# Optimization experiments

Measured on AMD Instinct MI355X. Metric: run time of the kernel, lower is better.

## Reference

```python
import jax, jax.numpy as jnp
import numpy as np


def setup_inputs() -> dict:
    key = jax.random.key(0)
    ks = jax.random.split(key, 4)
    B, N, C, S, D_AGG, D_OUT = 16, 2048, 128, 25, 128, 128
    # sparse binary adjacency, avg degree ~ N*0.01 ~ 20
    A = (jax.random.uniform(ks[0], (B, N, N)) < 0.01).astype(jnp.float32)
    X = jax.random.normal(ks[1], (B, N, C), dtype=jnp.float32)
    Wa = jax.random.normal(ks[2], (C, D_AGG), dtype=jnp.float32) * 0.05
    ba = jnp.zeros((D_AGG,), jnp.float32)
    Wc = jax.random.normal(ks[3], (C + D_AGG, D_OUT), dtype=jnp.float32) * 0.05
    bc = jnp.zeros((D_OUT,), jnp.float32)
    return {"A": A, "X": X, "Wa": Wa, "ba": ba, "Wc": Wc, "bc": bc, "n_samples": S}


def reference(A, X, Wa, ba, Wc, bc, n_samples):
    # Per node: take up to n_samples neighbors (nonzero adjacency entries).
    # Original randomly subsamples when degree > S; we take the first S by
    # index (lax.top_k is stable, ties -> lowest index). Missing slots are
    # zero rows, matching the original tf.pad: they contribute relu(ba) to
    # the max-aggregator, exactly like the padded/no-neighbor branches.
    mask = (A != 0).astype(X.dtype)                      # [B,N,N]
    vals, idx = jax.lax.top_k(mask, n_samples)           # [B,N,S]
    feats = jax.vmap(lambda x, i: jnp.take(x, i, axis=0))(X, idx)  # [B,N,S,C]
    feats = feats * vals[..., None]                      # zero padded slots
    # max aggregator: relu(neigh @ Wa + ba), max over sampled neighbors
    h = jax.nn.relu(jnp.einsum('bnsc,cd->bnsd', feats, Wa) + ba)
    agg = h.max(axis=2)                                  # [B,N,D_AGG]
    # concat self features with aggregated, project, relu
    cat = jnp.concatenate([X, agg], axis=-1)             # [B,N,C+D_AGG]
    out = jax.nn.relu(jnp.einsum('bnk,ko->bno', cat, Wc) + bc)  # [B,N,D_OUT]
    # per-graph Frobenius-norm normalization with div_no_nan semantics
    norm = jnp.sqrt(jnp.sum(out * out, axis=(1, 2), keepdims=True))
    return jnp.where(norm > 0, out / norm, jnp.zeros_like(out))
```

## Files before the change

### kernel.cpp

```cpp
#include <hip/hip_runtime.h>


typedef __attribute__((ext_vector_type(8))) short short8;
typedef __attribute__((ext_vector_type(4))) float f32x4;
typedef __attribute__((ext_vector_type(4))) float fvec4;
typedef unsigned int uint;
typedef unsigned short ushort;

__device__ __forceinline__ ushort f2bf(float x) {
    uint u = __builtin_bit_cast(uint, x);
    u += 0x7FFFu + ((u >> 16) & 1u);
    return (ushort)(u >> 16);
}
__device__ __forceinline__ float bflo(uint h) { uint v = h << 16;         return __builtin_bit_cast(float, v); }
__device__ __forceinline__ float bfhi(uint h) { uint v = h & 0xFFFF0000u; return __builtin_bit_cast(float, v); }

__global__ __launch_bounds__(256) void prep_w_k(
    const float* __restrict__ Wa, ushort* __restrict__ Wat,
    uint* __restrict__ ctr)
{
    int i = blockIdx.x * 256 + threadIdx.x;
    int d = i >> 7, k = i & 127;
    Wat[i] = f2bf(Wa[k * 128 + d]);
    if (i == 0) *ctr = 0u;
}

__device__ __forceinline__ void gemm_core(
    const float*  __restrict__ Xf, const ushort* __restrict__ A1,
    const ushort* __restrict__ Bt, int ktiles, int tile,
    ushort* Asm, ushort* Bsm, f32x4 acc[4][4])
{
    const int tid = threadIdx.x;
    const int l = tid & 63, w = tid >> 6;
    const int wm = (w >> 1) * 64, wn = (w & 1) * 64;
    const size_t row0 = (size_t)tile * 128;
    const int KT = ktiles << 7;

    for (int t = 0; t < ktiles; ++t) {
        __syncthreads();
        if (t == 0) {
#pragma unroll
            for (int j = 0; j < 8; ++j) {
                int gid = (j << 8) + tid;
                int r = gid >> 4, g = gid & 15;
                const float* s = Xf + (row0 + r) * 128 + g * 8;
                short8 pk;
#pragma unroll
                for (int e = 0; e < 8; ++e) pk[e] = (short)f2bf(s[e]);
                *(short8*)&Asm[r * 128 + ((g ^ (r & 7)) << 3)] = pk;
            }
        } else {
#pragma unroll
            for (int j = 0; j < 8; ++j) {
                int gid = (j << 8) + tid;
                int r = gid >> 4, g = gid & 15;
                short8 v = *(const short8*)(A1 + (row0 + r) * 128 + g * 8);
                *(short8*)&Asm[r * 128 + ((g ^ (r & 7)) << 3)] = v;
            }
        }
#pragma unroll
        for (int j = 0; j < 8; ++j) {
            int gid = (j << 8) + tid;
            int r = gid >> 4, g = gid & 15;
            short8 v = *(const short8*)(Bt + (size_t)r * KT + (t << 7) + g * 8);
            *(short8*)&Bsm[r * 128 + ((g ^ (r & 7)) << 3)] = v;
        }
        __syncthreads();
#pragma unroll
        for (int ks = 0; ks < 4; ++ks) {
            int gg = (ks << 2) + (l >> 4);
            short8 af[4], bfr[4];
#pragma unroll
            for (int m = 0; m < 4; ++m) {
                int r = wm + m * 16 + (l & 15);
                af[m] = *(const short8*)&Asm[r * 128 + ((gg ^ (r & 7)) << 3)];
            }
#pragma unroll
            for (int n = 0; n < 4; ++n) {
                int c = wn + n * 16 + (l & 15);
                bfr[n] = *(const short8*)&Bsm[c * 128 + ((gg ^ (c & 7)) << 3)];
            }
#pragma unroll
            for (int m = 0; m < 4; ++m)
#pragma unroll
                for (int n = 0; n < 4; ++n)
                    acc[m][n] = __builtin_amdgcn_mfma_f32_16x16x32_bf16(
                        af[m], bfr[n], acc[m][n], 0, 0, 0);
        }
    }
}

__global__ __launch_bounds__(256) void gemm_k1_k(
    const float* __restrict__ X, const ushort* __restrict__ Wat,
    const float* __restrict__ ba, ushort* __restrict__ H)
{
    __shared__ ushort Asm[128 * 128];
    __shared__ ushort Bsm[128 * 128];
    f32x4 acc[4][4] = {};
    gemm_core(X, nullptr, Wat, 1, blockIdx.x, Asm, Bsm, acc);

    const int tid = threadIdx.x, l = tid & 63, w = tid >> 6;
    const int wm = (w >> 1) * 64, wn = (w & 1) * 64;
    const size_t row0 = (size_t)blockIdx.x * 128;
    float bcol[4];
#pragma unroll
    for (int n = 0; n < 4; ++n) bcol[n] = ba[wn + n * 16 + (l & 15)];
#pragma unroll
    for (int m = 0; m < 4; ++m) {
        int rbase = wm + m * 16 + ((l >> 4) << 2);
#pragma unroll
        for (int n = 0; n < 4; ++n) {
            int col = wn + n * 16 + (l & 15);
#pragma unroll
            for (int r = 0; r < 4; ++r) {
                float v = fmaxf(acc[m][n][r] + bcol[n], 0.f);
                H[(row0 + rbase + r) * 128 + col] = f2bf(v);
            }
        }
    }
}

__global__ __launch_bounds__(256) void agg_k(
    const float* __restrict__ A,
    const uint*  __restrict__ Hu,
    const float* __restrict__ ba,
    uint* __restrict__ aggu,
    const int* __restrict__ nsp,
    const float* __restrict__ Wc,
    ushort* __restrict__ Wct)
{
    if (blockIdx.x >= 8192) {
        int j = (blockIdx.x - 8192) * 256 + threadIdx.x;
        int d = j >> 8, k = j & 255;
        Wct[j] = f2bf(Wc[k * 128 + d]);
        return;
    }

    __shared__ int idxs[4][32];
    const int l = threadIdx.x & 63;
    const int w = threadIdx.x >> 6;
    const int bid   = blockIdx.x;
    const int xcd   = bid & 7;
    const int grp   = bid >> 3;
    const int batch = ((grp >> 9) << 3) + xcd;
    const int node  = (batch << 11) + ((grp & 511) << 2) + w;
    int S = nsp[0]; if (S > 32) S = 32;

    const fvec4* rowp = (const fvec4*)(A + (size_t)node * 2048);
    fvec4 v[8];
#pragma unroll
    for (int c = 0; c < 8; ++c)
        v[c] = __builtin_nontemporal_load(rowp + c * 64 + l);

    const unsigned long long lt = (1ull << l) - 1ull;
    int base = 0;
#pragma unroll
    for (int c = 0; c < 8; ++c) {
        if (base < S) {
            unsigned long long m0 = __ballot(v[c][0] != 0.f);
            unsigned long long m1 = __ballot(v[c][1] != 0.f);
            unsigned long long m2 = __ballot(v[c][2] != 0.f);
            unsigned long long m3 = __ballot(v[c][3] != 0.f);
            int below = __popcll(m0 & lt) + __popcll(m1 & lt)
                      + __popcll(m2 & lt) + __popcll(m3 & lt);
            int o0 = (int)((m0 >> l) & 1), o1 = (int)((m1 >> l) & 1);
            int o2 = (int)((m2 >> l) & 1), o3 = (int)((m3 >> l) & 1);
            int r0 = base + below;
            int r1 = r0 + o0, r2 = r1 + o1, r3 = r2 + o2;
            int e = (c << 8) + (l << 2);
            if (o0 && r0 < S) idxs[w][r0] = e;
            if (o1 && r1 < S) idxs[w][r1] = e + 1;
            if (o2 && r2 < S) idxs[w][r2] = e + 2;
            if (o3 && r3 < S) idxs[w][r3] = e + 3;
            base += __popcll(m0) + __popcll(m1) + __popcll(m2) + __popcll(m3);
        }
    }
    int found = base < S ? base : S;

    float i0 = fmaxf(ba[2 * l], 0.f), i1 = fmaxf(ba[2 * l + 1], 0.f);
    float r0f = i0, r1f = i1;
    if (found > 0) {
        int fill = idxs[w][0];
        if (l < 32)
            idxs[w][l] = (l < found) ? idxs[w][l] : fill;

        const uint* HB = Hu + ((size_t)batch << 17);
        uint h[32];
#pragma unroll
        for (int q = 0; q < 32; ++q)
            h[q] = HB[(size_t)idxs[w][q] * 64 + l];

        float a0[8], a1[8];
#pragma unroll
        for (int q = 0; q < 8; ++q) { a0[q] = i0; a1[q] = i1; }
#pragma unroll
        for (int q = 0; q < 32; ++q) {
            a0[q & 7] = fmaxf(a0[q & 7], bflo(h[q]));
            a1[q & 7] = fmaxf(a1[q & 7], bfhi(h[q]));
        }
#pragma unroll
        for (int q = 0; q < 4; ++q) {
            a0[q] = fmaxf(a0[q], a0[q + 4]);
            a1[q] = fmaxf(a1[q], a1[q + 4]);
        }
        r0f = fmaxf(fmaxf(a0[0], a0[1]), fmaxf(a0[2], a0[3]));
        r1f = fmaxf(fmaxf(a1[0], a1[1]), fmaxf(a1[2], a1[3]));
    }
    aggu[(size_t)node * 64 + l] = (uint)f2bf(r0f) | ((uint)f2bf(r1f) << 16);
}

__global__ __launch_bounds__(256) void gemm_k3_k(
    const float* __restrict__ X, const ushort* __restrict__ agg,
    const ushort* __restrict__ Wct, const float* __restrict__ bc,
    float* __restrict__ out, float* __restrict__ partials,
    uint* __restrict__ ctr)
{
    __shared__ ushort Asm[128 * 128];
    __shared__ ushort Bsm[128 * 128];
    __shared__ float wred[4];
    __shared__ float ssc;
    f32x4 acc[4][4] = {};
    const int tile = blockIdx.x;
    gemm_core(X, agg, Wct, 2, tile, Asm, Bsm, acc);

    const int tid = threadIdx.x, l = tid & 63, w = tid >> 6;
    const int wm = (w >> 1) * 64, wn = (w & 1) * 64;
    const size_t row0 = (size_t)tile * 128;

    float bcol[4];
#pragma unroll
    for (int n = 0; n < 4; ++n) bcol[n] = bc[wn + n * 16 + (l & 15)];
    float lsum = 0.f;
#pragma unroll
    for (int m = 0; m < 4; ++m)
#pragma unroll
        for (int n = 0; n < 4; ++n)
#pragma unroll
            for (int r = 0; r < 4; ++r) {
                float v = fmaxf(acc[m][n][r] + bcol[n], 0.f);
                acc[m][n][r] = v;
                lsum += v * v;
            }
#pragma unroll
    for (int off = 32; off > 0; off >>= 1) lsum += __shfl_down(lsum, off);
    if (l == 0) wred[w] = lsum;
    __syncthreads();
    if (tid == 0) {
        partials[tile] = wred[0] + wred[1] + wred[2] + wred[3];
        __threadfence();
        __hip_atomic_fetch_add(ctr, 1u, __ATOMIC_ACQ_REL,
                               __HIP_MEMORY_SCOPE_AGENT);
        while (__hip_atomic_load(ctr, __ATOMIC_ACQUIRE,
                                 __HIP_MEMORY_SCOPE_AGENT) < 256u)
            __builtin_amdgcn_s_sleep(8);
        float s = 0.f;
        const int bb = tile >> 4;
#pragma unroll
        for (int i = 0; i < 16; ++i)
            s += __hip_atomic_load(&partials[bb * 16 + i], __ATOMIC_RELAXED,
                                   __HIP_MEMORY_SCOPE_AGENT);
        float norm = sqrtf(s);
        ssc = (norm > 0.f) ? (1.f / norm) : 0.f;
    }
    __syncthreads();
    const float sc = ssc;
#pragma unroll
    for (int m = 0; m < 4; ++m) {
        int rbase = wm + m * 16 + ((l >> 4) << 2);
#pragma unroll
        for (int n = 0; n < 4; ++n) {
            int col = wn + n * 16 + (l & 15);
#pragma unroll
            for (int r = 0; r < 4; ++r)
                out[(row0 + rbase + r) * 128 + col] = acc[m][n][r] * sc;
        }
    }
}

extern "C" void kernel_launch(void* const* d_in, const int* in_sizes, int n_in,
                              void* d_out, int out_size, void* d_ws, size_t ws_size,
                              hipStream_t stream) {
    const float* A  = (const float*)d_in[0];
    const float* X  = (const float*)d_in[1];
    const float* Wa = (const float*)d_in[2];
    const float* ba = (const float*)d_in[3];
    const float* Wc = (const float*)d_in[4];
    const float* bc = (const float*)d_in[5];
    const int*  nsp = (const int*)d_in[6];

    float* out = (float*)d_out;
    char* ws = (char*)d_ws;
    ushort* H        = (ushort*)ws;
    ushort* agg      = (ushort*)(ws + (8u << 20));
    ushort* Wat      = (ushort*)(ws + (16u << 20));
    ushort* Wct      = (ushort*)(ws + (16u << 20) + 32768);
    float*  partials = (float*) (ws + (16u << 20) + 131072);
    uint*   ctr      = (uint*)  (ws + (16u << 20) + 132096);

    prep_w_k<<<64, 256, 0, stream>>>(Wa, Wat, ctr);
    gemm_k1_k<<<256, 256, 0, stream>>>(X, Wat, ba, H);
    agg_k<<<8192 + 128, 256, 0, stream>>>(A, (const uint*)H, ba, (uint*)agg,
                                          nsp, Wc, Wct);
    gemm_k3_k<<<256, 256, 0, stream>>>(X, agg, Wct, bc, out, partials, ctr);
}
```

Before: 90.68 us.

## Fuse GEMM1, aggregation and GEMM2 into one persistent kernel with grid barriers

Replaces the three main kernels with a single persistent kernel of 512 blocks over 64-row tiles. Grid-wide atomic barriers separate the H projection, the neighbor max-aggregation and the output GEMM with norm. The aggregation now loops over 16 nodes per wave and prefetches the next adjacency row while gathering H. The aim is to remove launch gaps and tail effects, at the cost of fewer blocks streaming the 256MB adjacency (less memory-level parallelism) and three spin barriers.

```diff
diff --git a/kernel.cpp b/kernel.cpp
--- a/kernel.cpp
+++ b/kernel.cpp
@@ -15,32 +15,50 @@
 __device__ __forceinline__ float bflo(uint h) { uint v = h << 16;         return __builtin_bit_cast(float, v); }
 __device__ __forceinline__ float bfhi(uint h) { uint v = h & 0xFFFF0000u; return __builtin_bit_cast(float, v); }
 
-__global__ __launch_bounds__(256) void prep_w_k(
-    const float* __restrict__ Wa, ushort* __restrict__ Wat,
-    uint* __restrict__ ctr)
+__global__ __launch_bounds__(256) void prep_k(
+    const float* __restrict__ Wa, const float* __restrict__ Wc,
+    ushort* __restrict__ Wat, ushort* __restrict__ Wct, uint* __restrict__ ctr)
 {
     int i = blockIdx.x * 256 + threadIdx.x;
-    int d = i >> 7, k = i & 127;
-    Wat[i] = f2bf(Wa[k * 128 + d]);
-    if (i == 0) *ctr = 0u;
-}
-
-__device__ __forceinline__ void gemm_core(
+    if (i < 16384) {
+        int d = i >> 7, k = i & 127;
+        Wat[i] = f2bf(Wa[k * 128 + d]);
+    } else {
+        int j = i - 16384;
+        int d = j >> 8, k = j & 255;
+        Wct[j] = f2bf(Wc[k * 128 + d]);
+    }
+    if (blockIdx.x == 0 && threadIdx.x < 4) ctr[threadIdx.x] = 0u;
+}
+
+__device__ __forceinline__ void gbar(uint* c, int tid) {
+    __syncthreads();
+    if (tid == 0) {
+        __threadfence();
+        __hip_atomic_fetch_add(c, 1u, __ATOMIC_ACQ_REL,
+                               __HIP_MEMORY_SCOPE_AGENT);
+        while (__hip_atomic_load(c, __ATOMIC_ACQUIRE,
+                                 __HIP_MEMORY_SCOPE_AGENT) < 512u)
+            __builtin_amdgcn_s_sleep(4);
+    }
+    __syncthreads();
+    __threadfence();
+}
+
+__device__ __forceinline__ void gemm64(
     const float*  __restrict__ Xf, const ushort* __restrict__ A1,
-    const ushort* __restrict__ Bt, int ktiles, int tile,
-    ushort* Asm, ushort* Bsm, f32x4 acc[4][4])
+    const ushort* __restrict__ Bt, int KT, int ktiles, int tile64,
+    int tid, ushort* Asm, ushort* Bsm, f32x4 acc[4][2])
 {
-    const int tid = threadIdx.x;
     const int l = tid & 63, w = tid >> 6;
-    const int wm = (w >> 1) * 64, wn = (w & 1) * 64;
-    const size_t row0 = (size_t)tile * 128;
-    const int KT = ktiles << 7;
+    const int wn = w * 32;
+    const size_t row0 = (size_t)tile64 * 64;
 
     for (int t = 0; t < ktiles; ++t) {
         __syncthreads();
         if (t == 0) {
 #pragma unroll
-            for (int j = 0; j < 8; ++j) {
+            for (int j = 0; j < 4; ++j) {
                 int gid = (j << 8) + tid;
                 int r = gid >> 4, g = gid & 15;
                 const float* s = Xf + (row0 + r) * 128 + g * 8;
@@ -51,7 +69,7 @@
             }
         } else {
 #pragma unroll
-            for (int j = 0; j < 8; ++j) {
+            for (int j = 0; j < 4; ++j) {
                 int gid = (j << 8) + tid;
                 int r = gid >> 4, g = gid & 15;
                 short8 v = *(const short8*)(A1 + (row0 + r) * 128 + g * 8);
@@ -61,204 +79,191 @@
 #pragma unroll
         for (int j = 0; j < 8; ++j) {
             int gid = (j << 8) + tid;
-            int r = gid >> 4, g = gid & 15;
-            short8 v = *(const short8*)(Bt + (size_t)r * KT + (t << 7) + g * 8);
-            *(short8*)&Bsm[r * 128 + ((g ^ (r & 7)) << 3)] = v;
+            int c = gid >> 4, g = gid & 15;
+            short8 v = *(const short8*)(Bt + (size_t)c * KT + (t << 7) + g * 8);
+            *(short8*)&Bsm[c * 128 + ((g ^ (c & 7)) << 3)] = v;
         }
         __syncthreads();
 #pragma unroll
         for (int ks = 0; ks < 4; ++ks) {
             int gg = (ks << 2) + (l >> 4);
-            short8 af[4], bfr[4];
+            short8 af[4], bfr[2];
 #pragma unroll
             for (int m = 0; m < 4; ++m) {
-                int r = wm + m * 16 + (l & 15);
+                int r = m * 16 + (l & 15);
                 af[m] = *(const short8*)&Asm[r * 128 + ((gg ^ (r & 7)) << 3)];
             }
 #pragma unroll
-            for (int n = 0; n < 4; ++n) {
+            for (int n = 0; n < 2; ++n) {
                 int c = wn + n * 16 + (l & 15);
                 bfr[n] = *(const short8*)&Bsm[c * 128 + ((gg ^ (c & 7)) << 3)];
             }
 #pragma unroll
             for (int m = 0; m < 4; ++m)
 #pragma unroll
-                for (int n = 0; n < 4; ++n)
+                for (int n = 0; n < 2; ++n)
                     acc[m][n] = __builtin_amdgcn_mfma_f32_16x16x32_bf16(
                         af[m], bfr[n], acc[m][n], 0, 0, 0);
         }
     }
 }
 
-__global__ __launch_bounds__(256) void gemm_k1_k(
-    const float* __restrict__ X, const ushort* __restrict__ Wat,
-    const float* __restrict__ ba, ushort* __restrict__ H)
+__global__ __launch_bounds__(256, 2) void mega_k(
+    const float* __restrict__ A, const float* __restrict__ X,
+    const ushort* __restrict__ Wat, const ushort* __restrict__ Wct,
+    const float* __restrict__ ba, const float* __restrict__ bc,
+    ushort* __restrict__ H, uint* __restrict__ aggu,
+    float* __restrict__ out, float* __restrict__ partials,
+    uint* __restrict__ ctr, const int* __restrict__ nsp)
 {
-    __shared__ ushort Asm[128 * 128];
-    __shared__ ushort Bsm[128 * 128];
-    f32x4 acc[4][4] = {};
-    gemm_core(X, nullptr, Wat, 1, blockIdx.x, Asm, Bsm, acc);
-
-    const int tid = threadIdx.x, l = tid & 63, w = tid >> 6;
-    const int wm = (w >> 1) * 64, wn = (w & 1) * 64;
-    const size_t row0 = (size_t)blockIdx.x * 128;
-    float bcol[4];
-#pragma unroll
-    for (int n = 0; n < 4; ++n) bcol[n] = ba[wn + n * 16 + (l & 15)];
-#pragma unroll
-    for (int m = 0; m < 4; ++m) {
-        int rbase = wm + m * 16 + ((l >> 4) << 2);
-#pragma unroll
-        for (int n = 0; n < 4; ++n) {
-            int col = wn + n * 16 + (l & 15);
-#pragma unroll
-            for (int r = 0; r < 4; ++r) {
-                float v = fmaxf(acc[m][n][r] + bcol[n], 0.f);
-                H[(row0 + rbase + r) * 128 + col] = f2bf(v);
-            }
-        }
-    }
-}
-
-__global__ __launch_bounds__(256) void agg_k(
-    const float* __restrict__ A,
-    const uint*  __restrict__ Hu,
-    const float* __restrict__ ba,
-    uint* __restrict__ aggu,
-    const int* __restrict__ nsp,
-    const float* __restrict__ Wc,
-    ushort* __restrict__ Wct)
-{
-    if (blockIdx.x >= 8192) {
-        int j = (blockIdx.x - 8192) * 256 + threadIdx.x;
-        int d = j >> 8, k = j & 255;
-        Wct[j] = f2bf(Wc[k * 128 + d]);
-        return;
-    }
-
-    __shared__ int idxs[4][32];
-    const int l = threadIdx.x & 63;
-    const int w = threadIdx.x >> 6;
-    const int bid   = blockIdx.x;
-    const int xcd   = bid & 7;
-    const int grp   = bid >> 3;
-    const int batch = ((grp >> 9) << 3) + xcd;
-    const int node  = (batch << 11) + ((grp & 511) << 2) + w;
-    int S = nsp[0]; if (S > 32) S = 32;
-
-    const fvec4* rowp = (const fvec4*)(A + (size_t)node * 2048);
-    fvec4 v[8];
-#pragma unroll
-    for (int c = 0; c < 8; ++c)
-        v[c] = __builtin_nontemporal_load(rowp + c * 64 + l);
-
-    const unsigned long long lt = (1ull << l) - 1ull;
-    int base = 0;
-#pragma unroll
-    for (int c = 0; c < 8; ++c) {
-        if (base < S) {
-            unsigned long long m0 = __ballot(v[c][0] != 0.f);
-            unsigned long long m1 = __ballot(v[c][1] != 0.f);
-            unsigned long long m2 = __ballot(v[c][2] != 0.f);
-            unsigned long long m3 = __ballot(v[c][3] != 0.f);
-            int below = __popcll(m0 & lt) + __popcll(m1 & lt)
-                      + __popcll(m2 & lt) + __popcll(m3 & lt);
-            int o0 = (int)((m0 >> l) & 1), o1 = (int)((m1 >> l) & 1);
-            int o2 = (int)((m2 >> l) & 1), o3 = (int)((m3 >> l) & 1);
-            int r0 = base + below;
-            int r1 = r0 + o0, r2 = r1 + o1, r3 = r2 + o2;
-            int e = (c << 8) + (l << 2);
-            if (o0 && r0 < S) idxs[w][r0] = e;
-            if (o1 && r1 < S) idxs[w][r1] = e + 1;
-            if (o2 && r2 < S) idxs[w][r2] = e + 2;
-            if (o3 && r3 < S) idxs[w][r3] = e + 3;
-            base += __popcll(m0) + __popcll(m1) + __popcll(m2) + __popcll(m3);
-        }
-    }
-    int found = base < S ? base : S;
-
-    float i0 = fmaxf(ba[2 * l], 0.f), i1 = fmaxf(ba[2 * l + 1], 0.f);
-    float r0f = i0, r1f = i1;
-    if (found > 0) {
-        int fill = idxs[w][0];
-        if (l < 32)
-            idxs[w][l] = (l < found) ? idxs[w][l] : fill;
-
-        const uint* HB = Hu + ((size_t)batch << 17);
-        uint h[32];
-#pragma unroll
-        for (int q = 0; q < 32; ++q)
-            h[q] = HB[(size_t)idxs[w][q] * 64 + l];
-
-        float a0[8], a1[8];
-#pragma unroll
-        for (int q = 0; q < 8; ++q) { a0[q] = i0; a1[q] = i1; }
-#pragma unroll
-        for (int q = 0; q < 32; ++q) {
-            a0[q & 7] = fmaxf(a0[q & 7], bflo(h[q]));
-            a1[q & 7] = fmaxf(a1[q & 7], bfhi(h[q]));
-        }
-#pragma unroll
-        for (int q = 0; q < 4; ++q) {
-            a0[q] = fmaxf(a0[q], a0[q + 4]);
-            a1[q] = fmaxf(a1[q], a1[q + 4]);
-        }
-        r0f = fmaxf(fmaxf(a0[0], a0[1]), fmaxf(a0[2], a0[3]));
-        r1f = fmaxf(fmaxf(a1[0], a1[1]), fmaxf(a1[2], a1[3]));
-    }
-    aggu[(size_t)node * 64 + l] = (uint)f2bf(r0f) | ((uint)f2bf(r1f) << 16);
-}
-
-__global__ __launch_bounds__(256) void gemm_k3_k(
-    const float* __restrict__ X, const ushort* __restrict__ agg,
-    const ushort* __restrict__ Wct, const float* __restrict__ bc,
-    float* __restrict__ out, float* __restrict__ partials,
-    uint* __restrict__ ctr)
-{
-    __shared__ ushort Asm[128 * 128];
+    __shared__ ushort Asm[64 * 128];
     __shared__ ushort Bsm[128 * 128];
     __shared__ float wred[4];
     __shared__ float ssc;
-    f32x4 acc[4][4] = {};
-    const int tile = blockIdx.x;
-    gemm_core(X, agg, Wct, 2, tile, Asm, Bsm, acc);
 
     const int tid = threadIdx.x, l = tid & 63, w = tid >> 6;
-    const int wm = (w >> 1) * 64, wn = (w & 1) * 64;
-    const size_t row0 = (size_t)tile * 128;
-
-    float bcol[4];
-#pragma unroll
-    for (int n = 0; n < 4; ++n) bcol[n] = bc[wn + n * 16 + (l & 15)];
-    float lsum = 0.f;
-#pragma unroll
-    for (int m = 0; m < 4; ++m)
-#pragma unroll
-        for (int n = 0; n < 4; ++n)
-#pragma unroll
-            for (int r = 0; r < 4; ++r) {
-                float v = fmaxf(acc[m][n][r] + bcol[n], 0.f);
-                acc[m][n][r] = v;
-                lsum += v * v;
-            }
-#pragma unroll
-    for (int off = 32; off > 0; off >>= 1) lsum += __shfl_down(lsum, off);
-    if (l == 0) wred[w] = lsum;
-    __syncthreads();
+    const int bid = blockIdx.x;
+    const int xcd = bid & 7, rk = bid >> 3;
+    const int b_blk = (rk < 32) ? xcd : xcd + 8;
+    const int rk2 = rk & 31;
+    const int tile64 = b_blk * 32 + rk2;
+    const int wn = w * 32;
+    const size_t row0 = (size_t)tile64 * 64;
+
+    {
+        f32x4 acc[4][2] = {};
+        gemm64(X, nullptr, Wat, 128, 1, tile64, tid, Asm, Bsm, acc);
+        float bcol[2];
+#pragma unroll
+        for (int n = 0; n < 2; ++n) bcol[n] = ba[wn + n * 16 + (l & 15)];
+#pragma unroll
+        for (int m = 0; m < 4; ++m) {
+            int rbase = m * 16 + ((l >> 4) << 2);
+#pragma unroll
+            for (int n = 0; n < 2; ++n) {
+                int col = wn + n * 16 + (l & 15);
+#pragma unroll
+                for (int r = 0; r < 4; ++r)
+                    H[(row0 + rbase + r) * 128 + col] =
+                        f2bf(fmaxf(acc[m][n][r] + bcol[n], 0.f));
+            }
+        }
+    }
+    gbar(&ctr[0], tid);
+
+    {
+        int S = nsp[0]; if (S > 32) S = 32;
+        int* idxs = (int*)Asm;
+        const uint* HB = (const uint*)H + ((size_t)b_blk << 17);
+        const float i0 = fmaxf(ba[2 * l], 0.f), i1 = fmaxf(ba[2 * l + 1], 0.f);
+        const unsigned long long lt = (1ull << l) - 1ull;
+        const int nodeb = (b_blk << 11) + (rk2 << 6);
+
+        fvec4 v[8];
+        {
+            const fvec4* rp = (const fvec4*)(A + (size_t)(nodeb + w) * 2048);
+#pragma unroll
+            for (int c = 0; c < 8; ++c)
+                v[c] = __builtin_nontemporal_load(rp + c * 64 + l);
+        }
+        for (int i = 0; i < 16; ++i) {
+            const int node = nodeb + i * 4 + w;
+            int base = 0;
+#pragma unroll
+            for (int c = 0; c < 8; ++c) {
+                if (base < S) {
+                    unsigned long long m0 = __ballot(v[c][0] != 0.f);
+                    unsigned long long m1 = __ballot(v[c][1] != 0.f);
+                    unsigned long long m2 = __ballot(v[c][2] != 0.f);
+                    unsigned long long m3 = __ballot(v[c][3] != 0.f);
+                    int below = __popcll(m0 & lt) + __popcll(m1 & lt)
+                              + __popcll(m2 & lt) + __popcll(m3 & lt);
+                    int o0 = (int)((m0 >> l) & 1), o1 = (int)((m1 >> l) & 1);
+                    int o2 = (int)((m2 >> l) & 1), o3 = (int)((m3 >> l) & 1);
+                    int r0 = base + below;
+                    int r1 = r0 + o0, r2 = r1 + o1, r3 = r2 + o2;
+                    int e = (c << 8) + (l << 2);
+                    if (o0 && r0 < S) idxs[w * 32 + r0] = e;
+                    if (o1 && r1 < S) idxs[w * 32 + r1] = e + 1;
+                    if (o2 && r2 < S) idxs[w * 32 + r2] = e + 2;
+                    if (o3 && r3 < S) idxs[w * 32 + r3] = e + 3;
+                    base += __popcll(m0) + __popcll(m1)
+                          + __popcll(m2) + __popcll(m3);
+                }
+            }
+            const int found = base < S ? base : S;
+            const bool have = found > 0;
+
+            uint h[32];
+            if (have) {
+                int fill = idxs[w * 32];
+                if (l < 32)
+                    idxs[w * 32 + l] = (l < found) ? idxs[w * 32 + l] : fill;
+#pragma unroll
+                for (int q = 0; q < 32; ++q)
+                    h[q] = HB[(size_t)idxs[w * 32 + q] * 64 + l];
+            }
+            if (i < 15) {
+                const fvec4* rp =
+                    (const fvec4*)(A + (size_t)(nodeb + (i + 1) * 4 + w) * 2048);
+#pragma unroll
+                for (int c = 0; c < 8; ++c)
+                    v[c] = __builtin_nontemporal_load(rp + c * 64 + l);
+            }
+            float r0f = i0, r1f = i1;
+            if (have) {
+                float a0[8], a1[8];
+#pragma unroll
+                for (int q = 0; q < 8; ++q) { a0[q] = i0; a1[q] = i1; }
+#pragma unroll
+                for (int q = 0; q < 32; ++q) {
+                    a0[q & 7] = fmaxf(a0[q & 7], bflo(h[q]));
+                    a1[q & 7] = fmaxf(a1[q & 7], bfhi(h[q]));
+                }
+#pragma unroll
+                for (int q = 0; q < 4; ++q) {
+                    a0[q] = fmaxf(a0[q], a0[q + 4]);
+                    a1[q] = fmaxf(a1[q], a1[q + 4]);
+                }
+                r0f = fmaxf(fmaxf(a0[0], a0[1]), fmaxf(a0[2], a0[3]));
+                r1f = fmaxf(fmaxf(a1[0], a1[1]), fmaxf(a1[2], a1[3]));
+            }
+            aggu[(size_t)node * 64 + l] =
+                (uint)f2bf(r0f) | ((uint)f2bf(r1f) << 16);
+        }
+    }
+    gbar(&ctr[1], tid);
+
+    f32x4 acc[4][2] = {};
+    gemm64(X, (const ushort*)aggu, Wct, 256, 2, tile64, tid, Asm, Bsm, acc);
+    {
+        float bcol[2];
+#pragma unroll
+        for (int n = 0; n < 2; ++n) bcol[n] = bc[wn + n * 16 + (l & 15)];
+        float lsum = 0.f;
+#pragma unroll
+        for (int m = 0; m < 4; ++m)
+#pragma unroll
+            for (int n = 0; n < 2; ++n)
+#pragma unroll
+                for (int r = 0; r < 4; ++r) {
+                    float vv = fmaxf(acc[m][n][r] + bcol[n], 0.f);
+                    acc[m][n][r] = vv;
+                    lsum += vv * vv;
+                }
+#pragma unroll
+        for (int off = 32; off > 0; off >>= 1) lsum += __shfl_down(lsum, off);
+        if (l == 0) wred[w] = lsum;
+        __syncthreads();
+        if (tid == 0)
+            partials[tile64] = wred[0] + wred[1] + wred[2] + wred[3];
+    }
+    gbar(&ctr[2], tid);
+
     if (tid == 0) {
-        partials[tile] = wred[0] + wred[1] + wred[2] + wred[3];
-        __threadfence();
-        __hip_atomic_fetch_add(ctr, 1u, __ATOMIC_ACQ_REL,
-                               __HIP_MEMORY_SCOPE_AGENT);
-        while (__hip_atomic_load(ctr, __ATOMIC_ACQUIRE,
-                                 __HIP_MEMORY_SCOPE_AGENT) < 256u)
-            __builtin_amdgcn_s_sleep(8);
         float s = 0.f;
-        const int bb = tile >> 4;
-#pragma unroll
-        for (int i = 0; i < 16; ++i)
-            s += __hip_atomic_load(&partials[bb * 16 + i], __ATOMIC_RELAXED,
-                                   __HIP_MEMORY_SCOPE_AGENT);
+#pragma unroll
+        for (int i = 0; i < 32; ++i) s += partials[b_blk * 32 + i];
         float norm = sqrtf(s);
         ssc = (norm > 0.f) ? (1.f / norm) : 0.f;
     }
@@ -266,9 +271,9 @@
     const float sc = ssc;
 #pragma unroll
     for (int m = 0; m < 4; ++m) {
-        int rbase = wm + m * 16 + ((l >> 4) << 2);
-#pragma unroll
-        for (int n = 0; n < 4; ++n) {
+        int rbase = m * 16 + ((l >> 4) << 2);
+#pragma unroll
+        for (int n = 0; n < 2; ++n) {
             int col = wn + n * 16 + (l & 15);
 #pragma unroll
             for (int r = 0; r < 4; ++r)
@@ -291,15 +296,13 @@
     float* out = (float*)d_out;
     char* ws = (char*)d_ws;
     ushort* H        = (ushort*)ws;
-    ushort* agg      = (ushort*)(ws + (8u << 20));
+    uint*   agg      = (uint*)  (ws + (8u << 20));
     ushort* Wat      = (ushort*)(ws + (16u << 20));
     ushort* Wct      = (ushort*)(ws + (16u << 20) + 32768);
     float*  partials = (float*) (ws + (16u << 20) + 131072);
-    uint*   ctr      = (uint*)  (ws + (16u << 20) + 132096);
-
-    prep_w_k<<<64, 256, 0, stream>>>(Wa, Wat, ctr);
-    gemm_k1_k<<<256, 256, 0, stream>>>(X, Wat, ba, H);
-    agg_k<<<8192 + 128, 256, 0, stream>>>(A, (const uint*)H, ba, (uint*)agg,
-                                          nsp, Wc, Wct);
-    gemm_k3_k<<<256, 256, 0, stream>>>(X, agg, Wct, bc, out, partials, ctr);
-}
+    uint*   ctr      = (uint*)  (ws + (16u << 20) + 133120);
+
+    prep_k<<<192, 256, 0, stream>>>(Wa, Wc, Wat, Wct, ctr);
+    mega_k<<<512, 256, 0, stream>>>(A, X, Wat, Wct, ba, bc,
+                                    H, agg, out, partials, ctr, nsp);
+}
```

Measured after the change: 350.8 us. 287% more time.

## Split aggregation into independent scan and gather kernels, fold Wa transpose into GEMM

Applied to the files above, without the earlier changes.

Removes the separate weight-prep kernel by converting and transposing Wa directly inside the first GEMM. The fused aggregation kernel becomes two kernels. A scan kernel reads the adjacency and writes 16-bit global neighbor indices, with a sentinel row in H holding relu(ba) for nodes that have no neighbors. A gather kernel then does the max-reduction. The scan no longer depends on H, which may let the adjacency streaming run more independently of the first GEMM. The cost is an extra launch and an index buffer round-trip through memory.

```diff
diff --git a/kernel.cpp b/kernel.cpp
--- a/kernel.cpp
+++ b/kernel.cpp
@@ -15,93 +15,63 @@
 __device__ __forceinline__ float bflo(uint h) { uint v = h << 16;         return __builtin_bit_cast(float, v); }
 __device__ __forceinline__ float bfhi(uint h) { uint v = h & 0xFFFF0000u; return __builtin_bit_cast(float, v); }
 
-__global__ __launch_bounds__(256) void prep_w_k(
-    const float* __restrict__ Wa, ushort* __restrict__ Wat,
-    uint* __restrict__ ctr)
-{
-    int i = blockIdx.x * 256 + threadIdx.x;
-    int d = i >> 7, k = i & 127;
-    Wat[i] = f2bf(Wa[k * 128 + d]);
-    if (i == 0) *ctr = 0u;
-}
-
-__device__ __forceinline__ void gemm_core(
-    const float*  __restrict__ Xf, const ushort* __restrict__ A1,
-    const ushort* __restrict__ Bt, int ktiles, int tile,
-    ushort* Asm, ushort* Bsm, f32x4 acc[4][4])
-{
-    const int tid = threadIdx.x;
-    const int l = tid & 63, w = tid >> 6;
-    const int wm = (w >> 1) * 64, wn = (w & 1) * 64;
-    const size_t row0 = (size_t)tile * 128;
-    const int KT = ktiles << 7;
-
-    for (int t = 0; t < ktiles; ++t) {
-        __syncthreads();
-        if (t == 0) {
-#pragma unroll
-            for (int j = 0; j < 8; ++j) {
-                int gid = (j << 8) + tid;
-                int r = gid >> 4, g = gid & 15;
-                const float* s = Xf + (row0 + r) * 128 + g * 8;
-                short8 pk;
-#pragma unroll
-                for (int e = 0; e < 8; ++e) pk[e] = (short)f2bf(s[e]);
-                *(short8*)&Asm[r * 128 + ((g ^ (r & 7)) << 3)] = pk;
-            }
-        } else {
-#pragma unroll
-            for (int j = 0; j < 8; ++j) {
-                int gid = (j << 8) + tid;
-                int r = gid >> 4, g = gid & 15;
-                short8 v = *(const short8*)(A1 + (row0 + r) * 128 + g * 8);
-                *(short8*)&Asm[r * 128 + ((g ^ (r & 7)) << 3)] = v;
-            }
-        }
-#pragma unroll
-        for (int j = 0; j < 8; ++j) {
-            int gid = (j << 8) + tid;
-            int r = gid >> 4, g = gid & 15;
-            short8 v = *(const short8*)(Bt + (size_t)r * KT + (t << 7) + g * 8);
-            *(short8*)&Bsm[r * 128 + ((g ^ (r & 7)) << 3)] = v;
-        }
-        __syncthreads();
-#pragma unroll
-        for (int ks = 0; ks < 4; ++ks) {
-            int gg = (ks << 2) + (l >> 4);
-            short8 af[4], bfr[4];
-#pragma unroll
-            for (int m = 0; m < 4; ++m) {
-                int r = wm + m * 16 + (l & 15);
-                af[m] = *(const short8*)&Asm[r * 128 + ((gg ^ (r & 7)) << 3)];
-            }
-#pragma unroll
-            for (int n = 0; n < 4; ++n) {
-                int c = wn + n * 16 + (l & 15);
-                bfr[n] = *(const short8*)&Bsm[c * 128 + ((gg ^ (c & 7)) << 3)];
-            }
-#pragma unroll
-            for (int m = 0; m < 4; ++m)
-#pragma unroll
-                for (int n = 0; n < 4; ++n)
-                    acc[m][n] = __builtin_amdgcn_mfma_f32_16x16x32_bf16(
-                        af[m], bfr[n], acc[m][n], 0, 0, 0);
-        }
-    }
-}
-
 __global__ __launch_bounds__(256) void gemm_k1_k(
-    const float* __restrict__ X, const ushort* __restrict__ Wat,
+    const float* __restrict__ X, const float* __restrict__ Wa,
     const float* __restrict__ ba, ushort* __restrict__ H)
 {
     __shared__ ushort Asm[128 * 128];
     __shared__ ushort Bsm[128 * 128];
-    f32x4 acc[4][4] = {};
-    gemm_core(X, nullptr, Wat, 1, blockIdx.x, Asm, Bsm, acc);
-
     const int tid = threadIdx.x, l = tid & 63, w = tid >> 6;
     const int wm = (w >> 1) * 64, wn = (w & 1) * 64;
     const size_t row0 = (size_t)blockIdx.x * 128;
+
+#pragma unroll
+    for (int j = 0; j < 8; ++j) {
+        int gid = (j << 8) + tid;
+        int r = gid >> 4, g = gid & 15;
+        const float* s = X + (row0 + r) * 128 + g * 8;
+        short8 pk;
+#pragma unroll
+        for (int e = 0; e < 8; ++e) pk[e] = (short)f2bf(s[e]);
+        *(short8*)&Asm[r * 128 + ((g ^ (r & 7)) << 3)] = pk;
+    }
+    {
+        int c = tid >> 1;
+        int g0 = (tid & 1) * 8;
+#pragma unroll
+        for (int g = g0; g < g0 + 8; ++g) {
+            short8 pk;
+#pragma unroll
+            for (int e = 0; e < 8; ++e)
+                pk[e] = (short)f2bf(Wa[(size_t)(g * 8 + e) * 128 + c]);
+            *(short8*)&Bsm[c * 128 + ((g ^ (c & 7)) << 3)] = pk;
+        }
+    }
+    __syncthreads();
+
+    f32x4 acc[4][4] = {};
+#pragma unroll
+    for (int ks = 0; ks < 4; ++ks) {
+        int gg = (ks << 2) + (l >> 4);
+        short8 af[4], bfr[4];
+#pragma unroll
+        for (int m = 0; m < 4; ++m) {
+            int r = wm + m * 16 + (l & 15);
+            af[m] = *(const short8*)&Asm[r * 128 + ((gg ^ (r & 7)) << 3)];
+        }
+#pragma unroll
+        for (int n = 0; n < 4; ++n) {
+            int c = wn + n * 16 + (l & 15);
+            bfr[n] = *(const short8*)&Bsm[c * 128 + ((gg ^ (c & 7)) << 3)];
+        }
+#pragma unroll
+        for (int m = 0; m < 4; ++m)
+#pragma unroll
+            for (int n = 0; n < 4; ++n)
+                acc[m][n] = __builtin_amdgcn_mfma_f32_16x16x32_bf16(
+                    af[m], bfr[n], acc[m][n], 0, 0, 0);
+    }
+
     float bcol[4];
 #pragma unroll
     for (int n = 0; n < 4; ++n) bcol[n] = ba[wn + n * 16 + (l & 15)];
@@ -112,38 +82,39 @@
         for (int n = 0; n < 4; ++n) {
             int col = wn + n * 16 + (l & 15);
 #pragma unroll
-            for (int r = 0; r < 4; ++r) {
-                float v = fmaxf(acc[m][n][r] + bcol[n], 0.f);
-                H[(row0 + rbase + r) * 128 + col] = f2bf(v);
-            }
-        }
-    }
-}
-
-__global__ __launch_bounds__(256) void agg_k(
+            for (int r = 0; r < 4; ++r)
+                H[(row0 + rbase + r) * 128 + col] =
+                    f2bf(fmaxf(acc[m][n][r] + bcol[n], 0.f));
+        }
+    }
+    if (blockIdx.x == 0 && tid < 64) {
+        float a = fmaxf(ba[2 * tid], 0.f), b = fmaxf(ba[2 * tid + 1], 0.f);
+        ((uint*)(H + (size_t)32768 * 128))[tid] =
+            (uint)f2bf(a) | ((uint)f2bf(b) << 16);
+    }
+}
+
+__global__ __launch_bounds__(256) void scan_k(
     const float* __restrict__ A,
-    const uint*  __restrict__ Hu,
-    const float* __restrict__ ba,
-    uint* __restrict__ aggu,
+    ushort* __restrict__ idxg,
     const int* __restrict__ nsp,
     const float* __restrict__ Wc,
-    ushort* __restrict__ Wct)
+    ushort* __restrict__ Wct,
+    uint* __restrict__ ctr)
 {
     if (blockIdx.x >= 8192) {
         int j = (blockIdx.x - 8192) * 256 + threadIdx.x;
         int d = j >> 8, k = j & 255;
         Wct[j] = f2bf(Wc[k * 128 + d]);
+        if (blockIdx.x == 8192 && threadIdx.x == 0) *ctr = 0u;
         return;
     }
 
     __shared__ int idxs[4][32];
     const int l = threadIdx.x & 63;
     const int w = threadIdx.x >> 6;
-    const int bid   = blockIdx.x;
-    const int xcd   = bid & 7;
-    const int grp   = bid >> 3;
-    const int batch = ((grp >> 9) << 3) + xcd;
-    const int node  = (batch << 11) + ((grp & 511) << 2) + w;
+    const int node = blockIdx.x * 4 + w;
+    const int gbase = node & ~2047;
     int S = nsp[0]; if (S > 32) S = 32;
 
     const fvec4* rowp = (const fvec4*)(A + (size_t)node * 2048);
@@ -167,7 +138,7 @@
             int o2 = (int)((m2 >> l) & 1), o3 = (int)((m3 >> l) & 1);
             int r0 = base + below;
             int r1 = r0 + o0, r2 = r1 + o1, r3 = r2 + o2;
-            int e = (c << 8) + (l << 2);
+            int e = gbase + (c << 8) + (l << 2);
             if (o0 && r0 < S) idxs[w][r0] = e;
             if (o1 && r1 < S) idxs[w][r1] = e + 1;
             if (o2 && r2 < S) idxs[w][r2] = e + 2;
@@ -176,36 +147,52 @@
         }
     }
     int found = base < S ? base : S;
+    int fill = (found > 0) ? idxs[w][0] : 32768;
+    if (l < 32)
+        idxg[(size_t)node * 32 + l] =
+            (ushort)((l < found) ? idxs[w][l] : fill);
+}
+
+__global__ __launch_bounds__(256) void gather_k(
+    const ushort* __restrict__ idxg,
+    const uint*  __restrict__ Hu,
+    const float* __restrict__ ba,
+    uint* __restrict__ aggu)
+{
+    __shared__ ushort sidx[128];
+    const int l = threadIdx.x & 63;
+    const int w = threadIdx.x >> 6;
+    const int bid = blockIdx.x, xcd = bid & 7, grp = bid >> 3;
+    const int batch = ((grp >> 9) << 3) + xcd;
+    const int node0 = (batch << 11) + ((grp & 511) << 2);
+    const int node = node0 + w;
+
+    if (threadIdx.x < 64)
+        ((uint*)sidx)[threadIdx.x] =
+            ((const uint*)(idxg + (size_t)node0 * 32))[threadIdx.x];
+    __syncthreads();
+
+    uint h[32];
+#pragma unroll
+    for (int q = 0; q < 32; ++q)
+        h[q] = Hu[(size_t)sidx[w * 32 + q] * 64 + l];
 
     float i0 = fmaxf(ba[2 * l], 0.f), i1 = fmaxf(ba[2 * l + 1], 0.f);
-    float r0f = i0, r1f = i1;
-    if (found > 0) {
-        int fill = idxs[w][0];
-        if (l < 32)
-            idxs[w][l] = (l < found) ? idxs[w][l] : fill;
-
-        const uint* HB = Hu + ((size_t)batch << 17);
-        uint h[32];
-#pragma unroll
-        for (int q = 0; q < 32; ++q)
-            h[q] = HB[(size_t)idxs[w][q] * 64 + l];
-
-        float a0[8], a1[8];
-#pragma unroll
-        for (int q = 0; q < 8; ++q) { a0[q] = i0; a1[q] = i1; }
-#pragma unroll
-        for (int q = 0; q < 32; ++q) {
-            a0[q & 7] = fmaxf(a0[q & 7], bflo(h[q]));
-            a1[q & 7] = fmaxf(a1[q & 7], bfhi(h[q]));
-        }
-#pragma unroll
-        for (int q = 0; q < 4; ++q) {
-            a0[q] = fmaxf(a0[q], a0[q + 4]);
-            a1[q] = fmaxf(a1[q], a1[q + 4]);
-        }
-        r0f = fmaxf(fmaxf(a0[0], a0[1]), fmaxf(a0[2], a0[3]));
-        r1f = fmaxf(fmaxf(a1[0], a1[1]), fmaxf(a1[2], a1[3]));
-    }
+    float a0[8], a1[8];
+#pragma unroll
+    for (int q = 0; q < 8; ++q) { a0[q] = i0; a1[q] = i1; }
+#pragma unroll
+    for (int q = 0; q < 32; ++q) {
+        a0[q & 7] = fmaxf(a0[q & 7], bflo(h[q]));
+        a1[q & 7] = fmaxf(a1[q & 7], bfhi(h[q]));
+    }
+#pragma unroll
+    for (int q = 0; q < 4; ++q) {
+        a0[q] = fmaxf(a0[q], a0[q + 4]);
+        a1[q] = fmaxf(a1[q], a1[q + 4]);
+    }
+    float r0f = fmaxf(fmaxf(a0[0], a0[1]), fmaxf(a0[2], a0[3]));
+    float r1f = fmaxf(fmaxf(a1[0], a1[1]), fmaxf(a1[2], a1[3]));
     aggu[(size_t)node * 64 + l] = (uint)f2bf(r0f) | ((uint)f2bf(r1f) << 16);
 }
 
@@ -219,13 +206,64 @@
     __shared__ ushort Bsm[128 * 128];
     __shared__ float wred[4];
     __shared__ float ssc;
-    f32x4 acc[4][4] = {};
-    const int tile = blockIdx.x;
-    gemm_core(X, agg, Wct, 2, tile, Asm, Bsm, acc);
-
     const int tid = threadIdx.x, l = tid & 63, w = tid >> 6;
     const int wm = (w >> 1) * 64, wn = (w & 1) * 64;
+    const int tile = blockIdx.x;
     const size_t row0 = (size_t)tile * 128;
+
+    f32x4 acc[4][4] = {};
+    for (int t = 0; t < 2; ++t) {
+        __syncthreads();
+        if (t == 0) {
+#pragma unroll
+            for (int j = 0; j < 8; ++j) {
+                int gid = (j << 8) + tid;
+                int r = gid >> 4, g = gid & 15;
+                const float* s = X + (row0 + r) * 128 + g * 8;
+                short8 pk;
+#pragma unroll
+                for (int e = 0; e < 8; ++e) pk[e] = (short)f2bf(s[e]);
+                *(short8*)&Asm[r * 128 + ((g ^ (r & 7)) << 3)] = pk;
+            }
+        } else {
+#pragma unroll
+            for (int j = 0; j < 8; ++j) {
+                int gid = (j << 8) + tid;
+                int r = gid >> 4, g = gid & 15;
+                short8 v = *(const short8*)(agg + (row0 + r) * 128 + g * 8);
+                *(short8*)&Asm[r * 128 + ((g ^ (r & 7)) << 3)] = v;
+            }
+        }
+#pragma unroll
+        for (int j = 0; j < 8; ++j) {
+            int gid = (j << 8) + tid;
+            int r = gid >> 4, g = gid & 15;
+            short8 v = *(const short8*)(Wct + (size_t)r * 256 + (t << 7) + g * 8);
+            *(short8*)&Bsm[r * 128 + ((g ^ (r & 7)) << 3)] = v;
+        }
+        __syncthreads();
+#pragma unroll
+        for (int ks = 0; ks < 4; ++ks) {
+            int gg = (ks << 2) + (l >> 4);
+            short8 af[4], bfr[4];
+#pragma unroll
+            for (int m = 0; m < 4; ++m) {
+                int r = wm + m * 16 + (l & 15);
+                af[m] = *(const short8*)&Asm[r * 128 + ((gg ^ (r & 7)) << 3)];
+            }
+#pragma unroll
+            for (int n = 0; n < 4; ++n) {
+                int c = wn + n * 16 + (l & 15);
+                bfr[n] = *(const short8*)&Bsm[c * 128 + ((gg ^ (c & 7)) << 3)];
+            }
+#pragma unroll
+            for (int m = 0; m < 4; ++m)
+#pragma unroll
+                for (int n = 0; n < 4; ++n)
+                    acc[m][n] = __builtin_amdgcn_mfma_f32_16x16x32_bf16(
+                        af[m], bfr[n], acc[m][n], 0, 0, 0);
+        }
+    }
 
     float bcol[4];
 #pragma unroll
@@ -291,15 +329,14 @@
     float* out = (float*)d_out;
     char* ws = (char*)d_ws;
     ushort* H        = (ushort*)ws;
-    ushort* agg      = (ushort*)(ws + (8u << 20));
-    ushort* Wat      = (ushort*)(ws + (16u << 20));
-    ushort* Wct      = (ushort*)(ws + (16u << 20) + 32768);
-    float*  partials = (float*) (ws + (16u << 20) + 131072);
-    uint*   ctr      = (uint*)  (ws + (16u << 20) + 132096);
-
-    prep_w_k<<<64, 256, 0, stream>>>(Wa, Wat, ctr);
-    gemm_k1_k<<<256, 256, 0, stream>>>(X, Wat, ba, H);
-    agg_k<<<8192 + 128, 256, 0, stream>>>(A, (const uint*)H, ba, (uint*)agg,
-                                          nsp, Wc, Wct);
+    ushort* agg      = (ushort*)(ws + (9u << 20));
+    ushort* idxg     = (ushort*)(ws + (17u << 20));
+    ushort* Wct      = (ushort*)(ws + (19u << 20));
+    float*  partials = (float*) (ws + (19u << 20) + 65536);
+    uint*   ctr      = (uint*)  (ws + (19u << 20) + 66560);
+
+    gemm_k1_k<<<256, 256, 0, stream>>>(X, Wa, ba, H);
+    scan_k<<<8192 + 128, 256, 0, stream>>>(A, idxg, nsp, Wc, Wct, ctr);
+    gather_k<<<8192, 256, 0, stream>>>(idxg, (const uint*)H, ba, (uint*)agg);
     gemm_k3_k<<<256, 256, 0, stream>>>(X, agg, Wct, bc, out, partials, ctr);
 }
```

New measurement: 96.33 us. +6.2%, slower.
